# Kernel optimization log

Hardware: AMD Instinct MI355X
Metric: run time of the kernel (lower is better)

## Reference

```python
import jax, jax.numpy as jnp
import numpy as np

M1, M2 = 32, 32  # max_modes1, max_modes2
C_IN, C_OUT = 64, 64


def _neg_k(a):
    # torch.roll(torch.flip(a, dims=[-2,-1]), shifts=(1,1), dims=[-2,-1])
    return jnp.roll(jnp.flip(a, axis=(-2, -1)), shift=(1, 1), axis=(-2, -1))


def compl_mul2d(x1, x2):
    x1n = _neg_k(x1)
    x2n = _neg_k(x2)
    e = lambda a, b: jnp.einsum('bixy,ioxy->boxy', a, b)
    return 0.5 * (e(x1, x2) - e(x1n, x2n) + e(x1, x2n) + e(x1n, x2))


def setup_inputs() -> dict:
    key = jax.random.key(0)
    k1, k2, k3 = jax.random.split(key, 3)
    scale = 1.0 / (C_IN * C_OUT)
    return {
        "x": jax.random.normal(k1, (16, C_IN, 256, 256), dtype=jnp.float32),
        "weights1_re": scale * jax.random.uniform(k2, (C_IN, C_OUT, M1, M2), dtype=jnp.float32),
        "weights1_im": scale * jax.random.uniform(k3, (C_IN, C_OUT, M1, M2), dtype=jnp.float32),
        "error_estimate": 1,  # must be >= 1: smaller modes would break the einsum vs full weights
    }


def reference(x, weights1_re, weights1_im, error_estimate):
    B, Ci, H, W = x.shape
    modes1 = min(M1, max(1, int(M1 * error_estimate)))
    modes2 = min(M2, max(1, int(M2 * error_estimate)))
    weights1 = jax.lax.complex(weights1_re, weights1_im)  # complex64

    # spectral branch (computed exactly as in the original; note the original
    # module never uses out_ft in its return value)
    x_ft = jnp.fft.rfftn(x, axes=(2, 3))  # [B, Ci, H, W//2+1] complex64
    block = compl_mul2d(x_ft[:, :, :modes1, :modes2], weights1)
    out_ft = jnp.zeros((B, C_OUT, H, W // 2 + 1), dtype=jnp.complex64)
    out_ft = out_ft.at[:, :, :modes1, :modes2].set(block)

    # idht(x) with dim=None: fftn over ALL axes, (real+imag)/numel
    X = jnp.fft.fftn(x, axes=(0, 1, 2, 3))
    out = (X.real + X.imag) / x.size
    return out.astype(jnp.float32)
```

## Files before the change

kernel.cpp:

```cpp
#include <hip/hip_runtime.h>


#define NB 16
#define NC 64
#define NH 256
#define NW 256
#define WP 132
#define LSTRIDE (NH*WP)

__device__ __forceinline__ float2 cadd(float2 a, float2 b){ return make_float2(a.x+b.x, a.y+b.y); }
__device__ __forceinline__ float2 csub(float2 a, float2 b){ return make_float2(a.x-b.x, a.y-b.y); }
__device__ __forceinline__ float2 cmul(float2 a, float2 b){ return make_float2(a.x*b.x - a.y*b.y, a.x*b.y + a.y*b.x); }

__device__ __forceinline__ float2 twd(float frac){
  float sn, cs;
  __sincosf(-6.28318530717958647692f * frac, &sn, &cs);
  return make_float2(cs, sn);
}

__device__ __forceinline__ void dft4(float2&a,float2&b,float2&c,float2&d){
  float2 t0=cadd(a,c), t1=csub(a,c), t2=cadd(b,d), t3=csub(b,d);
  float2 t3i = make_float2(t3.y, -t3.x);
  a=cadd(t0,t2); c=csub(t0,t2); b=cadd(t1,t3i); d=csub(t1,t3i);
}

__device__ __forceinline__ void fft8(float2 v[8]){
  float2 e0=v[0],e1=v[2],e2=v[4],e3=v[6];
  float2 o0=v[1],o1=v[3],o2=v[5],o3=v[7];
  dft4(e0,e1,e2,e3); dft4(o0,o1,o2,o3);
  const float s=0.70710678118654752440f;
  float2 w1o=make_float2(s*(o1.x+o1.y), s*(o1.y-o1.x));
  float2 w2o=make_float2(o2.y, -o2.x);
  float2 w3o=make_float2(s*(o3.y-o3.x), -s*(o3.x+o3.y));
  v[0]=cadd(e0,o0); v[4]=csub(e0,o0);
  v[1]=cadd(e1,w1o); v[5]=csub(e1,w1o);
  v[2]=cadd(e2,w2o); v[6]=csub(e2,w2o);
  v[3]=cadd(e3,w3o); v[7]=csub(e3,w3o);
}

__device__ __forceinline__ void fft16(float2 v[16]){
  float2 e[8], o[8];
#pragma unroll
  for(int i=0;i<8;i++){ e[i]=v[2*i]; o[i]=v[2*i+1]; }
  fft8(e); fft8(o);
  const float c1=0.92387953251128675613f, s1=0.38268343236508977173f, s=0.70710678118654752440f;
  const float wr[8] = {1.f,  c1,  s,  s1, 0.f, -s1, -s, -c1};
  const float wi[8] = {0.f, -s1, -s, -c1, -1.f, -c1, -s, -s1};
#pragma unroll
  for(int k=0;k<8;k++){
    float2 wo = make_float2(wr[k]*o[k].x - wi[k]*o[k].y, wr[k]*o[k].y + wi[k]*o[k].x);
    v[k]=cadd(e[k],wo); v[k+8]=csub(e[k],wo);
  }
}

__global__ __launch_bounds__(256) void k1_fftW(const float* __restrict__ x, float2* __restrict__ S){
  __shared__ __align__(16) float smem[16*273*2];
  float2* lds2 = (float2*)smem;
  const int t    = threadIdx.x;
  const int j    = t & 15;
  const int line = t >> 4;
  const size_t gbase = (size_t)blockIdx.x * 16;

  const float4* xv = (const float4*)x;
#pragma unroll
  for(int r=0;r<4;r++){
    int f  = r*256 + t;
    int ln = f >> 6, pos = f & 63;
    float4 val = xv[(gbase + ln) * 64 + pos];
    *(float4*)(&smem[ln*264 + pos*4]) = val;
  }
  __syncthreads();

  float2 v[16];
#pragma unroll
  for(int n1=0;n1<16;n1++) v[n1] = make_float2(smem[line*264 + 16*n1 + j], 0.f);
  __syncthreads();

  fft16(v);
#pragma unroll
  for(int k1=0;k1<16;k1++){
    v[k1] = cmul(v[k1], twd((float)(j*k1) * (1.0f/256.0f)));
    lds2[line*273 + k1*17 + j] = v[k1];
  }
  __syncthreads();
  float2 u[16];
#pragma unroll
  for(int n2=0;n2<16;n2++) u[n2] = lds2[line*273 + j*17 + n2];
  fft16(u);
  float2* ps = S + (gbase + line) * WP;
#pragma unroll
  for(int k2=0;k2<8;k2++) ps[j + 16*k2] = u[k2];
  if(j==0) ps[128] = u[8];
}

__global__ __launch_bounds__(256) void k2_fftH(float2* __restrict__ S){
  __shared__ float2 lds[16*273];
  const int kwo  = threadIdx.x & 15;
  const int j    = threadIdx.x >> 4;
  const int tile = blockIdx.x % 9;
  const int slice= blockIdx.x / 9;
  const int kw   = tile*16 + kwo;
  const bool act = (kw <= 128);
  float2* base = S + (size_t)slice * NH * WP + kw;
  float2 v[16];
#pragma unroll
  for(int n1=0;n1<16;n1++) v[n1] = act ? base[(16*n1 + j) * WP] : make_float2(0.f,0.f);
  fft16(v);
#pragma unroll
  for(int k1=0;k1<16;k1++){
    v[k1] = cmul(v[k1], twd((float)(j*k1) * (1.0f/256.0f)));
    lds[kwo*273 + k1*17 + j] = v[k1];
  }
  __syncthreads();
  float2 u[16];
#pragma unroll
  for(int n2=0;n2<16;n2++) u[n2] = lds[kwo*273 + j*17 + n2];
  fft16(u);
  if(act){
#pragma unroll
    for(int k2=0;k2<16;k2++) base[(j + 16*k2) * WP] = u[k2];
  }
}

#define AIX(row,kwo) (((row)<<4) + ((kwo) ^ (((row)&7)<<1)))
__global__ __launch_bounds__(1024) void k3_fused(const float2* __restrict__ S, float* __restrict__ out){
  __shared__ __align__(16) float2 A[1024*16];
  const int t    = threadIdx.x;
  const int h    = blockIdx.x & 255;
  const int tile = blockIdx.x >> 8;
  const int kw0  = tile * 16;
  const float2* Sbase = S + (size_t)h * WP + kw0;

#pragma unroll
  for(int r=0;r<8;r++){
    int f    = t + 1024*r;
    int line = f >> 3;
    int part = f & 7;
    float4 val;
    if(kw0 + part*2 + 1 < WP){
      val = *(const float4*)(Sbase + (size_t)line * LSTRIDE + part*2);
    } else {
      val = make_float4(0.f,0.f,0.f,0.f);
    }
    *(float4*)(&A[AIX(line, part*2)]) = val;
  }
  __syncthreads();

#pragma unroll
  for(int q=0;q<2;q++){
    int item = t + 1024*q;
    int kwo = item & 15, n2 = (item>>4) & 7, b = item >> 7;
    float2 v[8];
#pragma unroll
    for(int n1=0;n1<8;n1++) v[n1] = A[AIX(b*64 + 8*n1 + n2, kwo)];
    fft8(v);
#pragma unroll
    for(int k1=0;k1<8;k1++) A[AIX(b*64 + 8*k1 + n2, kwo)] = cmul(v[k1], twd((float)(n2*k1) * (1.0f/64.0f)));
  }
  __syncthreads();

  {
    float2 u[2][8];
#pragma unroll
    for(int q=0;q<2;q++){
      int item = t + 1024*q;
      int kwo = item & 15, k1 = (item>>4) & 7, b = item >> 7;
#pragma unroll
      for(int n2=0;n2<8;n2++) u[q][n2] = A[AIX(b*64 + 8*k1 + n2, kwo)];
      fft8(u[q]);
    }
    __syncthreads();
#pragma unroll
    for(int q=0;q<2;q++){
      int item = t + 1024*q;
      int kwo = item & 15, k1 = (item>>4) & 7, b = item >> 7;
#pragma unroll
      for(int k2=0;k2<8;k2++) A[AIX(b*64 + (k1 + 8*k2), kwo)] = u[q][k2];
    }
  }
  __syncthreads();

  const float inv = 1.0f / 67108864.0f;
  const int h2 = (NH - h) & 255;
  {
    int kwo = t & 15, kc = t >> 4;
    float2 v[16];
#pragma unroll
    for(int b=0;b<16;b++) v[b] = A[AIX(b*64 + kc, kwo)];
    fft16(v);
    const int kw = kw0 + kwo;
    if(kw <= 128){
      const int kc2 = (NC - kc) & 63;
#pragma unroll
      for(int kb=0;kb<16;kb++){
        float2 z = v[kb];
        out[(((size_t)kb*NC + kc)*NH + h)*NW + kw] = (z.x + z.y) * inv;
        if(kw >= 1 && kw <= 127){
          const int kb2 = (16 - kb) & 15;
          out[(((size_t)kb2*NC + kc2)*NH + h2)*NW + (NW - kw)] = (z.x - z.y) * inv;
        }
      }
    }
  }
}

extern "C" void kernel_launch(void* const* d_in, const int* in_sizes, int n_in,
                              void* d_out, int out_size, void* d_ws, size_t ws_size,
                              hipStream_t stream) {
  const float* x = (const float*)d_in[0];
  float* out = (float*)d_out;
  float2* S  = (float2*)d_ws;

  k1_fftW<<<NB*NC*NH/16, 256,  0, stream>>>(x, S);
  k2_fftH<<<NB*NC*9,     256,  0, stream>>>(S);
  k3_fused<<<9*256,      1024, 0, stream>>>(S, out);
}
```

Before: 810.5 us.

## Restructure column FFT kernel with vectorized LDS-staged loads and separate Nyquist-column blocks

The H-direction FFT kernel now processes 32 columns per 512-thread block. It loads the 256x32 tile with coalesced float4 reads into LDS before transposing, instead of strided per-element global reads across 9 partially idle 16-column tiles. The Nyquist column (kw=128) is handled by a small set of extra blocks that each process 32 slices, which removes the mostly inactive ninth tile. This costs more LDS per block and an extra barrier, and may reduce occupancy.

```diff
diff --git a/kernel.cpp b/kernel.cpp
--- a/kernel.cpp
+++ b/kernel.cpp
@@ -93,32 +93,60 @@
   if(j==0) ps[128] = u[8];
 }
 
-__global__ __launch_bounds__(256) void k2_fftH(float2* __restrict__ S){
-  __shared__ float2 lds[16*273];
-  const int kwo  = threadIdx.x & 15;
-  const int j    = threadIdx.x >> 4;
-  const int tile = blockIdx.x % 9;
-  const int slice= blockIdx.x / 9;
-  const int kw   = tile*16 + kwo;
-  const bool act = (kw <= 128);
-  float2* base = S + (size_t)slice * NH * WP + kw;
-  float2 v[16];
-#pragma unroll
-  for(int n1=0;n1<16;n1++) v[n1] = act ? base[(16*n1 + j) * WP] : make_float2(0.f,0.f);
-  fft16(v);
-#pragma unroll
-  for(int k1=0;k1<16;k1++){
-    v[k1] = cmul(v[k1], twd((float)(j*k1) * (1.0f/256.0f)));
-    lds[kwo*273 + k1*17 + j] = v[k1];
-  }
-  __syncthreads();
-  float2 u[16];
-#pragma unroll
-  for(int n2=0;n2<16;n2++) u[n2] = lds[kwo*273 + j*17 + n2];
-  fft16(u);
-  if(act){
-#pragma unroll
-    for(int k2=0;k2<16;k2++) base[(j + 16*k2) * WP] = u[k2];
+__global__ __launch_bounds__(512) void k2_fftH(float2* __restrict__ S){
+  __shared__ __align__(16) float2 lds[8736];
+  const int t = threadIdx.x;
+  if(blockIdx.x < 4096){
+    const int tile  = blockIdx.x & 3;
+    const int slice = blockIdx.x >> 2;
+    float2* base = S + (size_t)slice * LSTRIDE + tile*32;
+
+#pragma unroll
+    for(int r=0;r<8;r++){
+      int f = t + 512*r;
+      int hh = f >> 4, p = f & 15;
+      float4 val = *(const float4*)(base + hh*WP + 2*p);
+      *(float4*)(&lds[hh*34 + 2*p]) = val;
+    }
+    __syncthreads();
+    const int c = t & 31, j = t >> 5;
+    float2 v[16];
+#pragma unroll
+    for(int n1=0;n1<16;n1++) v[n1] = lds[(16*n1 + j)*34 + c];
+    __syncthreads();
+    fft16(v);
+#pragma unroll
+    for(int k1=0;k1<16;k1++){
+      v[k1] = cmul(v[k1], twd((float)(j*k1) * (1.0f/256.0f)));
+      lds[c*273 + k1*17 + j] = v[k1];
+    }
+    __syncthreads();
+    float2 u[16];
+#pragma unroll
+    for(int n2=0;n2<16;n2++) u[n2] = lds[c*273 + j*17 + n2];
+    fft16(u);
+#pragma unroll
+    for(int k2=0;k2<16;k2++) base[(j + 16*k2)*WP + c] = u[k2];
+  } else {
+    const int s = t >> 4, j = t & 15;
+    const int slice0 = (blockIdx.x - 4096) * 32;
+    float2* base = S + (size_t)(slice0 + s) * LSTRIDE + 128;
+    float2 v[16];
+#pragma unroll
+    for(int n1=0;n1<16;n1++) v[n1] = base[(16*n1 + j)*WP];
+    fft16(v);
+#pragma unroll
+    for(int k1=0;k1<16;k1++){
+      v[k1] = cmul(v[k1], twd((float)(j*k1) * (1.0f/256.0f)));
+      lds[s*273 + k1*17 + j] = v[k1];
+    }
+    __syncthreads();
+    float2 u[16];
+#pragma unroll
+    for(int n2=0;n2<16;n2++) u[n2] = lds[s*273 + j*17 + n2];
+    fft16(u);
+#pragma unroll
+    for(int k2=0;k2<16;k2++) base[(j + 16*k2)*WP] = u[k2];
   }
 }
 
@@ -212,6 +240,6 @@
   float2* S  = (float2*)d_ws;
 
   k1_fftW<<<NB*NC*NH/16, 256,  0, stream>>>(x, S);
-  k2_fftH<<<NB*NC*9,     256,  0, stream>>>(S);
+  k2_fftH<<<4096+32,     512,  0, stream>>>(S);
   k3_fused<<<9*256,      1024, 0, stream>>>(S, out);
 }
```

New measurement: 833.1 us. 1.03x slower.
